# Optimization experiments

Hardware: AMD Instinct MI355X
Metric: run time of the kernel (lower is better)

## Reference

```python
import jax, jax.numpy as jnp
import numpy as np

EPS = 1e-6

def rms_norm(x, w):
    xf = x.astype(jnp.float32)
    xf = xf * jax.lax.rsqrt(jnp.mean(jnp.square(xf), axis=-1, keepdims=True) + EPS)
    return xf.astype(x.dtype) * w

def rotate_pairs(x):
    x = x.reshape(*x.shape[:-1], -1, 2)
    x1, x2 = x[..., 0], x[..., 1]
    return jnp.stack((-x2, x1), axis=-1).reshape(*x.shape[:-2], -1)

def apply_rope_axis(x, coords, inv_freq):
    # x: [B, H, T, axis_width]; coords: [T]; inv_freq: [axis_dim]
    angles = coords[:, None].astype(jnp.float32) * inv_freq[None, :]  # [T, axis_dim]
    cos = jnp.repeat(jnp.cos(angles), 2, axis=-1).astype(x.dtype)  # [T, axis_width]
    sin = jnp.repeat(jnp.sin(angles), 2, axis=-1).astype(x.dtype)
    return x * cos[None, None] + rotate_pairs(x) * sin[None, None]

def modulate(x, shift, scale):
    return x * (1.0 + scale[:, None, :]) + shift[:, None, :]

def setup_inputs() -> dict:
    key = jax.random.key(0)
    ks = jax.random.split(key, 16)
    B, T, D = 2, 2048, 1024
    HD = 64            # head_dim
    HID = 4096         # swiglu hidden (dim * mlp_ratio)
    CD = 1024          # cond_dim
    s = lambda n: 1.0 / np.sqrt(n)
    return {
        "x": jax.random.normal(ks[0], (B, T, D), jnp.float32),
        "cond": jax.random.normal(ks[1], (B, CD), jnp.float32),
        "norm1_w": jnp.ones((D,), jnp.float32),
        "qkv_w": jax.random.normal(ks[2], (3 * D, D), jnp.float32) * s(D),
        "q_norm_w": jnp.ones((HD,), jnp.float32),
        "k_norm_w": jnp.ones((HD,), jnp.float32),
        "proj_w": jax.random.normal(ks[3], (D, D), jnp.float32) * s(D),
        "proj_b": jnp.zeros((D,), jnp.float32),
        "norm2_w": jnp.ones((D,), jnp.float32),
        "fc1_w": jax.random.normal(ks[4], (2 * HID, D), jnp.float32) * s(D),
        "fc1_b": jnp.zeros((2 * HID,), jnp.float32),
        "fc2_w": jax.random.normal(ks[5], (D, HID), jnp.float32) * s(HID),
        "fc2_b": jnp.zeros((D,), jnp.float32),
        "ada_w": jax.random.normal(ks[6], (6 * D, CD), jnp.float32) * 0.02,
        "ada_b": jnp.zeros((6 * D,), jnp.float32),
        "height": 64,
        "width": 32,
    }

def reference(x, cond, norm1_w, qkv_w, q_norm_w, k_norm_w, proj_w, proj_b,
              norm2_w, fc1_w, fc1_b, fc2_w, fc2_b, ada_w, ada_b, height, width):
    B, T, D = x.shape
    HD = q_norm_w.shape[0]
    NH = D // HD
    scale = HD ** -0.5
    axis_dim = HD // 4
    axis_w = axis_dim * 2
    inv_freq = 1.0 / (10000.0 ** (jnp.arange(axis_dim, dtype=jnp.float32) / axis_dim))

    # AdaLN-Zero conditioning
    ada = jax.nn.silu(cond) @ ada_w.T + ada_b  # [B, 6D]
    sh_a, sc_a, g_a, sh_m, sc_m, g_m = jnp.split(ada, 6, axis=-1)

    # --- attention branch ---
    residual = x
    h = modulate(rms_norm(x, norm1_w), sh_a, sc_a)
    qkv = (h @ qkv_w.T).reshape(B, T, 3, NH, HD)
    q, k, v = qkv[:, :, 0], qkv[:, :, 1], qkv[:, :, 2]  # [B, T, NH, HD]
    q = rms_norm(q, q_norm_w)
    k = rms_norm(k, k_norm_w)
    q = q.transpose(0, 2, 1, 3)  # [B, NH, T, HD]
    k = k.transpose(0, 2, 1, 3)
    v = v.transpose(0, 2, 1, 3)

    # 2D RoPE: y coords on first axis_w dims, x coords on next axis_w dims
    yy, xx = jnp.meshgrid(jnp.arange(height), jnp.arange(width), indexing="ij")
    yy, xx = yy.reshape(-1), xx.reshape(-1)  # [T]
    q = jnp.concatenate([
        apply_rope_axis(q[..., :axis_w], yy, inv_freq),
        apply_rope_axis(q[..., axis_w:2 * axis_w], xx, inv_freq),
        q[..., 2 * axis_w:]], axis=-1)
    k = jnp.concatenate([
        apply_rope_axis(k[..., :axis_w], yy, inv_freq),
        apply_rope_axis(k[..., axis_w:2 * axis_w], xx, inv_freq),
        k[..., 2 * axis_w:]], axis=-1)

    attn = jax.nn.softmax(jnp.einsum("bhqd,bhkd->bhqk", q, k) * scale, axis=-1)
    h = jnp.einsum("bhqk,bhkd->bhqd", attn, v).transpose(0, 2, 1, 3).reshape(B, T, D)
    h = h @ proj_w.T + proj_b
    x = residual + g_a[:, None, :] * h

    # --- SwiGLU MLP branch ---
    residual = x
    h = modulate(rms_norm(x, norm2_w), sh_m, sc_m)
    value, gate = jnp.split(h @ fc1_w.T + fc1_b, 2, axis=-1)
    h = (value * jax.nn.silu(gate)) @ fc2_w.T + fc2_b
    return residual + g_m[:, None, :] * h
```

## Files before the change

kernel.cpp:

```cpp
#include <hip/hip_runtime.h>
#include <hip/hip_bf16.h>

#define B_   2
#define T_   2048
#define D_   1024
#define NH_  16
#define HD_  64
#define HID_ 4096
#define CD_  1024
#define SIX_D (6*D_)

typedef __bf16 bf16x8 __attribute__((ext_vector_type(8)));
typedef float  f32x4  __attribute__((ext_vector_type(4)));
typedef float  f32x16 __attribute__((ext_vector_type(16)));

__device__ __forceinline__ unsigned short f2bf(float f){
  union { float f; unsigned u; } v; v.f = f;
  unsigned r = v.u + 0x7FFFu + ((v.u >> 16) & 1u);
  return (unsigned short)(r >> 16);
}
__device__ __forceinline__ float bf2f(unsigned short u){
  union { unsigned x; float f; } v; v.x = ((unsigned)u) << 16; return v.f;
}

__device__ __forceinline__ void gl_lds16(const void* g, void* l){
  __builtin_amdgcn_global_load_lds(
      (__attribute__((address_space(1))) void*)const_cast<void*>(g),
      (__attribute__((address_space(3))) void*)l, 16, 0, 0);
}

__global__ void k_conv_all(const float* __restrict__ s0, const float* __restrict__ s1,
                           const float* __restrict__ s2, const float* __restrict__ s3,
                           unsigned short* __restrict__ d0, unsigned short* __restrict__ d1,
                           unsigned short* __restrict__ d2, unsigned short* __restrict__ d3){
  int bid = blockIdx.x;
  const float* s; unsigned short* d; int base;
  if (bid < 3072)      { s = s0; d = d0; base = bid; }
  else if (bid < 4096) { s = s1; d = d1; base = bid - 3072; }
  else if (bid < 12288){ s = s2; d = d2; base = bid - 4096; }
  else                 { s = s3; d = d3; base = bid - 12288; }
  int i = base*256 + threadIdx.x;
  float4 v = reinterpret_cast<const float4*>(s)[i];
  ushort4 o;
  o.x = f2bf(v.x); o.y = f2bf(v.y); o.z = f2bf(v.z); o.w = f2bf(v.w);
  reinterpret_cast<ushort4*>(d)[i] = o;
}

__global__ void k_ada(const float* __restrict__ cond, const float* __restrict__ ada_w,
                      const float* __restrict__ ada_b, float* __restrict__ ada){
  __shared__ float sc[CD_];
  int b = blockIdx.y;
  int tid = threadIdx.x;
  for (int i = tid; i < CD_; i += 256){
    float c = cond[b*CD_ + i];
    sc[i] = c / (1.f + __expf(-c));
  }
  __syncthreads();
  int wave = tid >> 6, lane = tid & 63;
  int colbase = blockIdx.x*64 + wave*16;
  #pragma unroll
  for (int c = 0; c < 16; c++){
    int col = colbase + c;
    const float* wr = ada_w + (size_t)col*CD_;
    float acc = 0.f;
    #pragma unroll
    for (int i = 0; i < 16; i++)
      acc += sc[lane + 64*i] * wr[lane + 64*i];
    #pragma unroll
    for (int m = 32; m > 0; m >>= 1) acc += __shfl_xor(acc, m, 64);
    if (lane == 0) ada[b*SIX_D + col] = acc + ada_b[col];
  }
}

__global__ void k_norm_mod(const float* __restrict__ x, const float* __restrict__ w,
                           const float* __restrict__ ada, int sh_off, int sc_off,
                           unsigned short* __restrict__ out){
  int row = blockIdx.x;
  int b = row >> 11;
  int tid = threadIdx.x;
  float4 xv = reinterpret_cast<const float4*>(x + (size_t)row*D_)[tid];
  float ss = xv.x*xv.x + xv.y*xv.y + xv.z*xv.z + xv.w*xv.w;
  #pragma unroll
  for (int m = 32; m > 0; m >>= 1) ss += __shfl_xor(ss, m, 64);
  __shared__ float red[4];
  int wave = tid >> 6;
  if ((tid & 63) == 0) red[wave] = ss;
  __syncthreads();
  float tot = red[0]+red[1]+red[2]+red[3];
  float rn = rsqrtf(tot * (1.f/(float)D_) + 1e-6f);
  float4 wv  = reinterpret_cast<const float4*>(w)[tid];
  float4 scv = reinterpret_cast<const float4*>(ada + b*SIX_D + sc_off)[tid];
  float4 shv = reinterpret_cast<const float4*>(ada + b*SIX_D + sh_off)[tid];
  ushort4 o;
  o.x = f2bf(xv.x*rn*wv.x*(1.f+scv.x)+shv.x);
  o.y = f2bf(xv.y*rn*wv.y*(1.f+scv.y)+shv.y);
  o.z = f2bf(xv.z*rn*wv.z*(1.f+scv.z)+shv.z);
  o.w = f2bf(xv.w*rn*wv.w*(1.f+scv.w)+shv.w);
  reinterpret_cast<ushort4*>(out + (size_t)row*D_)[tid] = o;
}

enum { EPI_F32 = 0, EPI_RESID = 1, EPI_BF16 = 2 };

template<int EPI>
__launch_bounds__(256)
__global__ void k_gemm_bt(const unsigned short* __restrict__ A,
                          const unsigned short* __restrict__ W,
                          int M, int N, int K,
                          void* __restrict__ outp,
                          const float* __restrict__ resid,
                          const float* __restrict__ ada, int g_off,
                          const float* __restrict__ bias){
  __shared__ __align__(16) unsigned short As[3][128*32];
  __shared__ __align__(16) unsigned short Bs[3][128*32];
  const int tid = threadIdx.x;
  const int wave = tid >> 6, lane = tid & 63;
  const int wm = (wave >> 1)*64, wn = (wave & 1)*64;
  const int m0 = blockIdx.y*128, n0 = blockIdx.x*128;
  const int fr = lane & 15, fq = lane >> 4;
  const int sl = (fq ^ ((fr >> 1) & 3))*8;
  const int r0 = tid >> 2, c0 = tid & 3;
  const int g0 = c0 ^ ((r0 >> 1) & 3);
  const int r1 = r0 + 64;
  const int g1 = c0 ^ ((r1 >> 1) & 3);
  const unsigned short* gA0 = A + (size_t)(m0 + r0)*K + g0*8;
  const unsigned short* gA1 = A + (size_t)(m0 + r1)*K + g1*8;
  const unsigned short* gB0 = W + (size_t)(n0 + r0)*K + g0*8;
  const unsigned short* gB1 = W + (size_t)(n0 + r1)*K + g1*8;
  const int l0 = (tid & ~63)*8, l1 = ((256 + tid) & ~63)*8;
  f32x4 acc[4][4] = {};
  auto stage = [&](int buf){
    gl_lds16(gA0, &As[buf][l0]);
    gl_lds16(gA1, &As[buf][l1]);
    gl_lds16(gB0, &Bs[buf][l0]);
    gl_lds16(gB1, &Bs[buf][l1]);
    gA0 += 32; gA1 += 32; gB0 += 32; gB1 += 32;
  };
  stage(0); stage(1); stage(2);
  const int NK = K >> 5;
  int cur = 0;
  for (int t = 0; t < NK; t++){
    if (t < NK - 2)      asm volatile("s_waitcnt vmcnt(8)" ::: "memory");
    else if (t < NK - 1) asm volatile("s_waitcnt vmcnt(4)" ::: "memory");
    else                 asm volatile("s_waitcnt vmcnt(0)" ::: "memory");
    __builtin_amdgcn_s_barrier();
    bf16x8 af[4], bfr[4];
    #pragma unroll
    for (int i = 0; i < 4; i++){
      af[i]  = *(const bf16x8*)&As[cur][(wm + i*16 + fr)*32 + sl];
      bfr[i] = *(const bf16x8*)&Bs[cur][(wn + i*16 + fr)*32 + sl];
    }
    __builtin_amdgcn_s_setprio(1);
    #pragma unroll
    for (int i = 0; i < 4; i++)
      #pragma unroll
      for (int j = 0; j < 4; j++)
        acc[i][j] = __builtin_amdgcn_mfma_f32_16x16x32_bf16(af[i], bfr[j], acc[i][j], 0,0,0);
    __builtin_amdgcn_s_setprio(0);
    __builtin_amdgcn_s_barrier();
    if (t + 3 < NK) stage(cur);
    cur = (cur == 2) ? 0 : cur + 1;
  }
  #pragma unroll
  for (int i = 0; i < 4; i++){
    #pragma unroll
    for (int j = 0; j < 4; j++){
      int col = n0 + wn + j*16 + fr;
      #pragma unroll
      for (int r = 0; r < 4; r++){
        int row = m0 + wm + i*16 + fq*4 + r;
        float v = acc[i][j][r];
        if (EPI == EPI_F32){
          ((float*)outp)[(size_t)row*N + col] = v;
        } else if (EPI == EPI_BF16){
          ((unsigned short*)outp)[(size_t)row*N + col] = f2bf(v);
        } else {
          int b = row >> 11;
          float g = ada[b*SIX_D + g_off + col];
          ((float*)outp)[(size_t)row*N + col] = resid[(size_t)row*N + col] + g*(v + bias[col]);
        }
      }
    }
  }
}

template<int EPI>
__launch_bounds__(256)
__global__ void k_gemm_bt64(const unsigned short* __restrict__ A,
                            const unsigned short* __restrict__ W,
                            int M, int N, int K,
                            void* __restrict__ outp,
                            const float* __restrict__ resid,
                            const float* __restrict__ ada, int g_off,
                            const float* __restrict__ bias){
  __shared__ __align__(16) unsigned short As[3][64*32];
  __shared__ __align__(16) unsigned short Bs[3][128*32];
  const int tid = threadIdx.x;
  const int wave = tid >> 6, lane = tid & 63;
  const int wm = (wave >> 1)*32, wn = (wave & 1)*64;
  const int m0 = blockIdx.y*64, n0 = blockIdx.x*128;
  const int fr = lane & 15, fq = lane >> 4;
  const int sl = (fq ^ ((fr >> 1) & 3))*8;
  const int r0 = tid >> 2, c0 = tid & 3;
  const int g0 = c0 ^ ((r0 >> 1) & 3);
  const int r1 = r0 + 64;
  const int g1 = c0 ^ ((r1 >> 1) & 3);
  const unsigned short* gA0 = A + (size_t)(m0 + r0)*K + g0*8;
  const unsigned short* gB0 = W + (size_t)(n0 + r0)*K + g0*8;
  const unsigned short* gB1 = W + (size_t)(n0 + r1)*K + g1*8;
  const int l0 = (tid & ~63)*8, l1 = ((256 + tid) & ~63)*8;
  f32x4 acc[2][4] = {};
  auto stage = [&](int buf){
    gl_lds16(gA0, &As[buf][l0]);
    gl_lds16(gB0, &Bs[buf][l0]);
    gl_lds16(gB1, &Bs[buf][l1]);
    gA0 += 32; gB0 += 32; gB1 += 32;
  };
  stage(0); stage(1); stage(2);
  const int NK = K >> 5;
  int cur = 0;
  for (int t = 0; t < NK; t++){
    if (t < NK - 2)      asm volatile("s_waitcnt vmcnt(6)" ::: "memory");
    else if (t < NK - 1) asm volatile("s_waitcnt vmcnt(3)" ::: "memory");
    else                 asm volatile("s_waitcnt vmcnt(0)" ::: "memory");
    __builtin_amdgcn_s_barrier();
    bf16x8 af[2], bfr[4];
    #pragma unroll
    for (int i = 0; i < 2; i++)
      af[i]  = *(const bf16x8*)&As[cur][(wm + i*16 + fr)*32 + sl];
    #pragma unroll
    for (int j = 0; j < 4; j++)
      bfr[j] = *(const bf16x8*)&Bs[cur][(wn + j*16 + fr)*32 + sl];
    __builtin_amdgcn_s_setprio(1);
    #pragma unroll
    for (int i = 0; i < 2; i++)
      #pragma unroll
      for (int j = 0; j < 4; j++)
        acc[i][j] = __builtin_amdgcn_mfma_f32_16x16x32_bf16(af[i], bfr[j], acc[i][j], 0,0,0);
    __builtin_amdgcn_s_setprio(0);
    __builtin_amdgcn_s_barrier();
    if (t + 3 < NK) stage(cur);
    cur = (cur == 2) ? 0 : cur + 1;
  }
  #pragma unroll
  for (int i = 0; i < 2; i++){
    #pragma unroll
    for (int j = 0; j < 4; j++){
      int col = n0 + wn + j*16 + fr;
      #pragma unroll
      for (int r = 0; r < 4; r++){
        int row = m0 + wm + i*16 + fq*4 + r;
        float v = acc[i][j][r];
        if (EPI == EPI_F32){
          ((float*)outp)[(size_t)row*N + col] = v;
        } else if (EPI == EPI_BF16){
          ((unsigned short*)outp)[(size_t)row*N + col] = f2bf(v);
        } else {
          int b = row >> 11;
          float g = ada[b*SIX_D + g_off + col];
          ((float*)outp)[(size_t)row*N + col] = resid[(size_t)row*N + col] + g*(v + bias[col]);
        }
      }
    }
  }
}

__launch_bounds__(256)
__global__ void k_gemm_fc1(const unsigned short* __restrict__ A,
                           const unsigned short* __restrict__ W,
                           const float* __restrict__ bias,
                           unsigned short* __restrict__ out){
  __shared__ __align__(16) unsigned short As[2][128*32];
  __shared__ __align__(16) unsigned short Bv[2][64*32];
  __shared__ __align__(16) unsigned short Bg[2][64*32];
  const int K = D_;
  const int tid = threadIdx.x;
  const int wave = tid >> 6, lane = tid & 63;
  const int wm = (wave >> 1)*64, wn = (wave & 1)*32;
  const int m0 = blockIdx.y*128, n0 = blockIdx.x*64;
  const int fr = lane & 15, fq = lane >> 4;
  const int sl = (fq ^ ((fr >> 1) & 3))*8;
  const int r0 = tid >> 2, c0 = tid & 3;
  const int g0 = c0 ^ ((r0 >> 1) & 3);
  const int r1 = r0 + 64;
  const int g1 = c0 ^ ((r1 >> 1) & 3);
  const unsigned short* gA0 = A + (size_t)(m0 + r0)*K + g0*8;
  const unsigned short* gA1 = A + (size_t)(m0 + r1)*K + g1*8;
  const unsigned short* gBv = W + (size_t)(n0 + r0)*K + g0*8;
  const unsigned short* gBg = W + (size_t)(HID_ + n0 + r0)*K + g0*8;
  const int l0 = (tid & ~63)*8, l1 = ((256 + tid) & ~63)*8;
  f32x4 accv[4][2] = {}, accg[4][2] = {};
  auto stage = [&](int buf){
    gl_lds16(gA0, &As[buf][l0]);
    gl_lds16(gA1, &As[buf][l1]);
    gl_lds16(gBv, &Bv[buf][l0]);
    gl_lds16(gBg, &Bg[buf][l0]);
    gA0 += 32; gA1 += 32; gBv += 32; gBg += 32;
  };
  stage(0); stage(1);
  const int NK = K >> 5;
  for (int t = 0; t < NK; t++){
    const int cur = t & 1;
    if (t < NK - 1) asm volatile("s_waitcnt vmcnt(4)" ::: "memory");
    else            asm volatile("s_waitcnt vmcnt(0)" ::: "memory");
    __builtin_amdgcn_s_barrier();
    bf16x8 af[4], bv[2], bg[2];
    #pragma unroll
    for (int i = 0; i < 4; i++)
      af[i] = *(const bf16x8*)&As[cur][(wm + i*16 + fr)*32 + sl];
    #pragma unroll
    for (int j = 0; j < 2; j++){
      bv[j] = *(const bf16x8*)&Bv[cur][(wn + j*16 + fr)*32 + sl];
      bg[j] = *(const bf16x8*)&Bg[cur][(wn + j*16 + fr)*32 + sl];
    }
    __builtin_amdgcn_s_setprio(1);
    #pragma unroll
    for (int i = 0; i < 4; i++)
      #pragma unroll
      for (int j = 0; j < 2; j++){
        accv[i][j] = __builtin_amdgcn_mfma_f32_16x16x32_bf16(af[i], bv[j], accv[i][j], 0,0,0);
        accg[i][j] = __builtin_amdgcn_mfma_f32_16x16x32_bf16(af[i], bg[j], accg[i][j], 0,0,0);
      }
    __builtin_amdgcn_s_setprio(0);
    __builtin_amdgcn_s_barrier();
    if (t + 2 < NK) stage(cur);
  }
  #pragma unroll
  for (int i = 0; i < 4; i++){
    #pragma unroll
    for (int j = 0; j < 2; j++){
      int col = n0 + wn + j*16 + fr;
      #pragma unroll
      for (int r = 0; r < 4; r++){
        int row = m0 + wm + i*16 + fq*4 + r;
        float vv = accv[i][j][r] + bias[col];
        float gg = accg[i][j][r] + bias[HID_ + col];
        float h = vv * (gg / (1.f + __expf(-gg)));
        out[(size_t)row*HID_ + col] = f2bf(h);
      }
    }
  }
}

__global__ void k_qkv_post(const unsigned short* __restrict__ qkv,
                           const float* __restrict__ qw, const float* __restrict__ kw,
                           const int* __restrict__ wptr,
                           unsigned short* __restrict__ q, unsigned short* __restrict__ k){
  int idx = blockIdx.x*4 + (threadIdx.x >> 6);
  int h = idx & (NH_-1);
  int t = (idx >> 4) & (T_-1);
  int b = idx >> 15;
  int d = threadIdx.x & 63;
  const unsigned short* base = qkv + (size_t)(b*T_ + t)*3072;
  float qv = bf2f(base[h*64 + d]);
  float kv = bf2f(base[1024 + h*64 + d]);
  float sq = qv*qv, sk = kv*kv;
  #pragma unroll
  for (int m = 32; m > 0; m >>= 1){ sq += __shfl_xor(sq, m, 64); sk += __shfl_xor(sk, m, 64); }
  qv *= rsqrtf(sq*(1.f/64.f) + 1e-6f) * qw[d];
  kv *= rsqrtf(sk*(1.f/64.f) + 1e-6f) * kw[d];
  int width = wptr[0];
  int yy = t / width, xx = t - yy*width;
  int coord = (d < 32) ? yy : xx;
  int fi = (d & 31) >> 1;
  float ifreq = __expf(-(float)fi * (9.210340371976184f/16.f));
  float ang = (float)coord * ifreq;
  float cs = cosf(ang), sn = sinf(ang);
  float pq = __shfl_xor(qv, 1, 64);
  float pk = __shfl_xor(kv, 1, 64);
  float rq = (d & 1) ? pq : -pq;
  float rk = (d & 1) ? pk : -pk;
  qv = qv*cs + rq*sn;
  kv = kv*cs + rk*sn;
  size_t o = ((size_t)(b*NH_ + h)*T_ + t)*64 + d;
  q[o] = f2bf(qv); k[o] = f2bf(kv);
}

__global__ void k_vtrans(const unsigned short* __restrict__ qkv, unsigned short* __restrict__ vt){
  __shared__ __align__(16) unsigned short TT[64*64];
  int bh = blockIdx.y, t0 = blockIdx.x*64;
  int b = bh >> 4, h = bh & 15;
  int tid = threadIdx.x;
  #pragma unroll
  for (int it = 0; it < 2; it++){
    int i2 = it*256 + tid;
    int t = i2 >> 3, c8 = (i2 & 7)*8;
    union { uint4 v; unsigned short u[8]; } ld;
    ld.v = *(const uint4*)(qkv + (size_t)(b*T_ + t0 + t)*3072 + 2048 + h*64 + c8);
    #pragma unroll
    for (int e = 0; e < 8; e++){
      int c = c8 + e;
      int gp = (t >> 3) ^ ((c >> 2) & 7);
      TT[c*64 + gp*8 + (t & 7)] = ld.u[e];
    }
  }
  __syncthreads();
  #pragma unroll
  for (int it = 0; it < 2; it++){
    int i2 = it*256 + tid;
    int d = i2 >> 3, g = i2 & 7;
    int gp = g ^ ((d >> 2) & 7);
    *(uint4*)(vt + ((size_t)(bh*64 + d)*T_ + t0 + g*8)) = *(const uint4*)&TT[d*64 + gp*8];
  }
}

__launch_bounds__(128, 2)
__global__ void k_attn(const unsigned short* __restrict__ q,
                       const unsigned short* __restrict__ k,
                       const unsigned short* __restrict__ vt,
                       unsigned short* __restrict__ out){
  __shared__ __align__(16) unsigned short Kl[2][64*64];
  __shared__ __align__(16) unsigned short Vl[2][64*64];
  const int tid  = threadIdx.x;
  const int wave = tid >> 6;
  const int lane = tid & 63;
  const int ln   = lane & 31;
  const int hi   = lane >> 5;
  const int id = blockIdx.x;
  const int bh = id & 31;
  const int q0 = (id >> 5)*64 + wave*32;

  bf16x8 qf[4];
  {
    const unsigned short* qp = q + ((size_t)bh*T_ + q0 + ln)*HD_ + hi*8;
    #pragma unroll
    for (int kk = 0; kk < 4; kk++)
      qf[kk] = *(const bf16x8*)(qp + kk*16);
  }

  const unsigned short* kp[4];
  const unsigned short* vp[4];
  int ldst[4];
  {
    const unsigned short* kg = k  + (size_t)bh*T_*HD_;
    const unsigned short* vg = vt + (size_t)bh*HD_*T_;
    #pragma unroll
    for (int rr = 0; rr < 4; rr++){
      int idx = rr*128 + tid;
      int row = idx >> 3, c = idx & 7;
      int g = c ^ (row & 7);
      kp[rr] = kg + (size_t)row*HD_ + g*8;
      vp[rr] = vg + (size_t)row*T_  + g*8;
      ldst[rr] = (idx & ~63)*8;
    }
  }
  auto stage = [&](int buf){
    #pragma unroll
    for (int rr = 0; rr < 4; rr++){
      gl_lds16(kp[rr], &Kl[buf][ldst[rr]]);
      gl_lds16(vp[rr], &Vl[buf][ldst[rr]]);
      kp[rr] += 64*HD_;
      vp[rr] += 64;
    }
  };

  f32x16 o0 = {}, o1 = {};
  float ls[4] = {};
  const int vr0 = ln*64, vr1 = (32 + ln)*64;
  const int sw = ln & 7;

  stage(0);
  asm volatile("s_waitcnt vmcnt(0)" ::: "memory");
  __builtin_amdgcn_s_barrier();

  for (int t = 0; t < T_/64; t++){
    const int cur = t & 1, nxt = cur ^ 1;
    if (t + 1 < T_/64){
      stage(nxt);
      asm volatile("s_waitcnt vmcnt(8)" ::: "memory");
    } else {
      asm volatile("s_waitcnt vmcnt(0)" ::: "memory");
    }
    __builtin_amdgcn_s_barrier();
    const unsigned short* Kc = Kl[cur];
    const unsigned short* Vc = Vl[cur];
    #pragma unroll
    for (int s2 = 0; s2 < 2; s2++){
      bf16x8 kf[4];
      const int kb = (s2*32 + ln)*64;
      #pragma unroll
      for (int kk = 0; kk < 4; kk++){
        int ch = (kk*2 + hi) ^ sw;
        kf[kk] = *(const bf16x8*)&Kc[kb + ch*8];
      }
      f32x16 sa = {}, sb = {};
      __builtin_amdgcn_s_setprio(1);
      sa = __builtin_amdgcn_mfma_f32_32x32x16_bf16(kf[0], qf[0], sa, 0, 0, 0);
      sb = __builtin_amdgcn_mfma_f32_32x32x16_bf16(kf[1], qf[1], sb, 0, 0, 0);
      sa = __builtin_amdgcn_mfma_f32_32x32x16_bf16(kf[2], qf[2], sa, 0, 0, 0);
      sb = __builtin_amdgcn_mfma_f32_32x32x16_bf16(kf[3], qf[3], sb, 0, 0, 0);
      __builtin_amdgcn_s_setprio(0);
      union { uint2 u2[2]; bf16x8 v; } v0f[2], v1f[2];
      #pragma unroll
      for (int c = 0; c < 2; c++){
        int chA = (s2*4 + c*2)     ^ sw;
        int chB = (s2*4 + c*2 + 1) ^ sw;
        v0f[c].u2[0] = *(const uint2*)&Vc[vr0 + chA*8 + hi*4];
        v0f[c].u2[1] = *(const uint2*)&Vc[vr0 + chB*8 + hi*4];
        v1f[c].u2[0] = *(const uint2*)&Vc[vr1 + chA*8 + hi*4];
        v1f[c].u2[1] = *(const uint2*)&Vc[vr1 + chB*8 + hi*4];
      }
      f32x16 sv = sa + sb;
      float p[16];
      #pragma unroll
      for (int r = 0; r < 16; r++)
        p[r] = __expf(fminf(sv[r]*0.125f, 30.f));
      union { __bf16 h[16]; bf16x8 v[2]; } pa;
      #pragma unroll
      for (int r = 0; r < 16; r++){
        pa.h[r] = (__bf16)p[r];
        ls[r & 3] += p[r];
      }
      __builtin_amdgcn_s_setprio(1);
      o0 = __builtin_amdgcn_mfma_f32_32x32x16_bf16(pa.v[0], v0f[0].v, o0, 0, 0, 0);
      o1 = __builtin_amdgcn_mfma_f32_32x32x16_bf16(pa.v[0], v1f[0].v, o1, 0, 0, 0);
      o0 = __builtin_amdgcn_mfma_f32_32x32x16_bf16(pa.v[1], v0f[1].v, o0, 0, 0, 0);
      o1 = __builtin_amdgcn_mfma_f32_32x32x16_bf16(pa.v[1], v1f[1].v, o1, 0, 0, 0);
      __builtin_amdgcn_s_setprio(0);
    }
    __builtin_amdgcn_s_barrier();
  }

  float lsum = ls[0] + ls[1] + ls[2] + ls[3];
  lsum += __shfl_xor(lsum, 32, 64);
  float inv = 1.f / lsum;
  const int b = bh >> 4, h = bh & 15;
  unsigned short* ob = out + ((size_t)(b*T_ + q0))*D_ + h*64 + ln;
  #pragma unroll
  for (int r = 0; r < 16; r++){
    int qr = (r & 3) + 8*(r >> 2) + 4*hi;
    float invr = __shfl(inv, qr, 64);
    unsigned short* op = ob + (size_t)qr*D_;
    op[0]  = f2bf(o0[r]*invr);
    op[32] = f2bf(o1[r]*invr);
  }
}

extern "C" void kernel_launch(void* const* d_in, const int* in_sizes, int n_in,
                              void* d_out, int out_size, void* d_ws, size_t ws_size,
                              hipStream_t stream){
  const float* x      = (const float*)d_in[0];
  const float* cond   = (const float*)d_in[1];
  const float* norm1w = (const float*)d_in[2];
  const float* qkv_w  = (const float*)d_in[3];
  const float* q_nw   = (const float*)d_in[4];
  const float* k_nw   = (const float*)d_in[5];
  const float* proj_w = (const float*)d_in[6];
  const float* proj_b = (const float*)d_in[7];
  const float* norm2w = (const float*)d_in[8];
  const float* fc1_w  = (const float*)d_in[9];
  const float* fc1_b  = (const float*)d_in[10];
  const float* fc2_w  = (const float*)d_in[11];
  const float* fc2_b  = (const float*)d_in[12];
  const float* ada_w  = (const float*)d_in[13];
  const float* ada_b  = (const float*)d_in[14];
  const int*   wptr   = (const int*)d_in[16];
  float* out = (float*)d_out;

  char* ws = (char*)d_ws;
  size_t off = 0;
  auto alloc = [&](size_t bytes)->void*{
    void* p = ws + off; off += (bytes + 255) & ~(size_t)255; return p;
  };
  unsigned short* w_qkv  = (unsigned short*)alloc(3072ull*1024*2);
  unsigned short* w_proj = (unsigned short*)alloc(1024ull*1024*2);
  unsigned short* w_fc1  = (unsigned short*)alloc(8192ull*1024*2);
  unsigned short* w_fc2  = (unsigned short*)alloc(1024ull*4096*2);
  float* ada             = (float*)alloc((size_t)B_*SIX_D*4);
  unsigned short* h1     = (unsigned short*)alloc(4096ull*1024*2);
  char* R                = (char*)alloc(4096ull*3072*4);
  unsigned short* qkv_out= (unsigned short*)R;
  unsigned short* attn_o = (unsigned short*)R;
  float* x1              = (float*)(R + (size_t)B_*T_*D_*2);
  unsigned short* qb     = (unsigned short*)alloc(32ull*2048*64*2);
  unsigned short* kb     = (unsigned short*)alloc(32ull*2048*64*2);
  unsigned short* vt     = (unsigned short*)alloc(32ull*64*2048*2);
  unsigned short* mlp    = (unsigned short*)alloc(4096ull*4096*2);
  (void)ws_size; (void)in_sizes; (void)n_in; (void)out_size;

  k_conv_all<<<16384, 256, 0, stream>>>(qkv_w, proj_w, fc1_w, fc2_w, w_qkv, w_proj, w_fc1, w_fc2);

  k_ada<<<dim3(SIX_D/64, B_), 256, 0, stream>>>(cond, ada_w, ada_b, ada);
  k_norm_mod<<<B_*T_, 256, 0, stream>>>(x, norm1w, ada, 0, D_, h1);
  k_gemm_bt<EPI_BF16><<<dim3(3072/128, 4096/128), 256, 0, stream>>>(
      h1, w_qkv, B_*T_, 3*D_, D_, qkv_out, nullptr, nullptr, 0, nullptr);
  k_qkv_post<<<B_*T_*NH_/4, 256, 0, stream>>>(qkv_out, q_nw, k_nw, wptr, qb, kb);
  k_vtrans<<<dim3(T_/64, 32), 256, 0, stream>>>(qkv_out, vt);
  k_attn<<<1024, 128, 0, stream>>>(qb, kb, vt, attn_o);
  k_gemm_bt64<EPI_RESID><<<dim3(1024/128, 4096/64), 256, 0, stream>>>(
      attn_o, w_proj, B_*T_, D_, D_, x1, x, ada, 2*D_, proj_b);
  k_norm_mod<<<B_*T_, 256, 0, stream>>>(x1, norm2w, ada, 3*D_, 4*D_, h1);
  k_gemm_fc1<<<dim3(HID_/64, 4096/128), 256, 0, stream>>>(h1, w_fc1, fc1_b, mlp);
  k_gemm_bt64<EPI_RESID><<<dim3(1024/128, 4096/64), 256, 0, stream>>>(
      mlp, w_fc2, B_*T_, D_, HID_, out, x1, ada, 5*D_, fc2_b);
}
```

Baseline: 467.8 us.

## Split-K the fc2 GEMM into two halves with a separate residual epilogue kernel

Replaces the single fc2 GEMM (K=4096, 512 blocks) with a split-K version that runs twice as many blocks, each covering half of K, with a 3-stage LDS pipeline. The partial results go into two fp32 buffers that reuse workspace regions, and a new finishing kernel sums them and applies bias, gate and residual. This targets low occupancy and the long serial K loop on a chip with many CUs, at the cost of extra fp32 partial writes and reads plus one more kernel launch.

```diff
diff --git a/kernel.cpp b/kernel.cpp
--- a/kernel.cpp
+++ b/kernel.cpp
@@ -265,6 +265,97 @@
 }
 
 __launch_bounds__(256)
+__global__ void k_gemm_fc2sk(const unsigned short* __restrict__ A,
+                             const unsigned short* __restrict__ W,
+                             float* __restrict__ p0, float* __restrict__ p1){
+  __shared__ __align__(16) unsigned short As[3][64*32];
+  __shared__ __align__(16) unsigned short Bs[3][128*32];
+  const int K = HID_, N = D_;
+  const int tid = threadIdx.x;
+  const int wave = tid >> 6, lane = tid & 63;
+  const int wm = (wave >> 1)*32, wn = (wave & 1)*64;
+  const int half = blockIdx.y & 1;
+  const int m0 = (blockIdx.y >> 1)*64, n0 = blockIdx.x*128;
+  const int kof = half*(HID_/2);
+  float* outp = half ? p1 : p0;
+  const int fr = lane & 15, fq = lane >> 4;
+  const int sl = (fq ^ ((fr >> 1) & 3))*8;
+  const int r0 = tid >> 2, c0 = tid & 3;
+  const int g0 = c0 ^ ((r0 >> 1) & 3);
+  const int r1 = r0 + 64;
+  const int g1 = c0 ^ ((r1 >> 1) & 3);
+  const unsigned short* gA0 = A + (size_t)(m0 + r0)*K + kof + g0*8;
+  const unsigned short* gB0 = W + (size_t)(n0 + r0)*K + kof + g0*8;
+  const unsigned short* gB1 = W + (size_t)(n0 + r1)*K + kof + g1*8;
+  const int l0 = (tid & ~63)*8, l1 = ((256 + tid) & ~63)*8;
+  f32x4 acc[2][4] = {};
+  auto stage = [&](int buf){
+    gl_lds16(gA0, &As[buf][l0]);
+    gl_lds16(gB0, &Bs[buf][l0]);
+    gl_lds16(gB1, &Bs[buf][l1]);
+    gA0 += 32; gB0 += 32; gB1 += 32;
+  };
+  stage(0); stage(1); stage(2);
+  const int NK = (HID_/2) >> 5;
+  int cur = 0;
+  for (int t = 0; t < NK; t++){
+    if (t < NK - 2)      asm volatile("s_waitcnt vmcnt(6)" ::: "memory");
+    else if (t < NK - 1) asm volatile("s_waitcnt vmcnt(3)" ::: "memory");
+    else                 asm volatile("s_waitcnt vmcnt(0)" ::: "memory");
+    __builtin_amdgcn_s_barrier();
+    bf16x8 af[2], bfr[4];
+    #pragma unroll
+    for (int i = 0; i < 2; i++)
+      af[i]  = *(const bf16x8*)&As[cur][(wm + i*16 + fr)*32 + sl];
+    #pragma unroll
+    for (int j = 0; j < 4; j++)
+      bfr[j] = *(const bf16x8*)&Bs[cur][(wn + j*16 + fr)*32 + sl];
+    __builtin_amdgcn_s_setprio(1);
+    #pragma unroll
+    for (int i = 0; i < 2; i++)
+      #pragma unroll
+      for (int j = 0; j < 4; j++)
+        acc[i][j] = __builtin_amdgcn_mfma_f32_16x16x32_bf16(af[i], bfr[j], acc[i][j], 0,0,0);
+    __builtin_amdgcn_s_setprio(0);
+    __builtin_amdgcn_s_barrier();
+    if (t + 3 < NK) stage(cur);
+    cur = (cur == 2) ? 0 : cur + 1;
+  }
+  #pragma unroll
+  for (int i = 0; i < 2; i++){
+    #pragma unroll
+    for (int j = 0; j < 4; j++){
+      int col = n0 + wn + j*16 + fr;
+      #pragma unroll
+      for (int r = 0; r < 4; r++){
+        int row = m0 + wm + i*16 + fq*4 + r;
+        outp[(size_t)row*N + col] = acc[i][j][r];
+      }
+    }
+  }
+}
+
+__global__ void k_fc2_fin(const float* __restrict__ p0, const float* __restrict__ p1,
+                          const float* __restrict__ resid, const float* __restrict__ ada,
+                          const float* __restrict__ bias, float* __restrict__ out){
+  int row = blockIdx.x;
+  int b = row >> 11;
+  int tid = threadIdx.x;
+  size_t base = (size_t)row*D_;
+  float4 a  = reinterpret_cast<const float4*>(p0 + base)[tid];
+  float4 c  = reinterpret_cast<const float4*>(p1 + base)[tid];
+  float4 rv = reinterpret_cast<const float4*>(resid + base)[tid];
+  float4 gv = reinterpret_cast<const float4*>(ada + b*SIX_D + 5*D_)[tid];
+  float4 bv = reinterpret_cast<const float4*>(bias)[tid];
+  float4 o;
+  o.x = rv.x + gv.x*(a.x + c.x + bv.x);
+  o.y = rv.y + gv.y*(a.y + c.y + bv.y);
+  o.z = rv.z + gv.z*(a.z + c.z + bv.z);
+  o.w = rv.w + gv.w*(a.w + c.w + bv.w);
+  reinterpret_cast<float4*>(out + base)[tid] = o;
+}
+
+__launch_bounds__(256)
 __global__ void k_gemm_fc1(const unsigned short* __restrict__ A,
                            const unsigned short* __restrict__ W,
                            const float* __restrict__ bias,
@@ -571,10 +662,12 @@
   unsigned short* qkv_out= (unsigned short*)R;
   unsigned short* attn_o = (unsigned short*)R;
   float* x1              = (float*)(R + (size_t)B_*T_*D_*2);
+  float* p0              = (float*)(R + (size_t)B_*T_*D_*2 + (size_t)B_*T_*D_*4);
   unsigned short* qb     = (unsigned short*)alloc(32ull*2048*64*2);
   unsigned short* kb     = (unsigned short*)alloc(32ull*2048*64*2);
   unsigned short* vt     = (unsigned short*)alloc(32ull*64*2048*2);
   unsigned short* mlp    = (unsigned short*)alloc(4096ull*4096*2);
+  float* p1              = (float*)qb;
   (void)ws_size; (void)in_sizes; (void)n_in; (void)out_size;
 
   k_conv_all<<<16384, 256, 0, stream>>>(qkv_w, proj_w, fc1_w, fc2_w, w_qkv, w_proj, w_fc1, w_fc2);
@@ -590,6 +683,6 @@
       attn_o, w_proj, B_*T_, D_, D_, x1, x, ada, 2*D_, proj_b);
   k_norm_mod<<<B_*T_, 256, 0, stream>>>(x1, norm2w, ada, 3*D_, 4*D_, h1);
   k_gemm_fc1<<<dim3(HID_/64, 4096/128), 256, 0, stream>>>(h1, w_fc1, fc1_b, mlp);
-  k_gemm_bt64<EPI_RESID><<<dim3(1024/128, 4096/64), 256, 0, stream>>>(
-      mlp, w_fc2, B_*T_, D_, HID_, out, x1, ada, 5*D_, fc2_b);
-}
+  k_gemm_fc2sk<<<dim3(1024/128, (4096/64)*2), 256, 0, stream>>>(mlp, w_fc2, p0, p1);
+  k_fc2_fin<<<B_*T_, 256, 0, stream>>>(p0, p1, x1, ada, fc2_b, out);
+}
```

After: 475.2 us. About the same (+1.6%).
